# Performance work log

Measured on AMD Instinct MI355X. Metric: run time of the kernel, lower is better.

## Reference

```python
import jax, jax.numpy as jnp
import numpy as np

B = 256          # graphs
NPG = 512        # nodes per graph
N = B * NPG      # 131072 nodes
DEG = 16
E = N * DEG      # 2097152 edges
EPG = E // B
EMB = 256
EF = 8
HID = 32
LATENT = [HID, HID, HID, 1]
TOTAL = sum(LATENT)          # 97
K = 30
S = 5            # max_seq_len
V = 5000         # num_vocab
NT = 100         # node types
ND = 20          # max depth
C1, C2, KW2 = 16, 32, 5
DENSE = ((K - 2) // 2 + 1 - KW2 + 1) * C2  # 352


def glorot(key, shape):
    fan_in, fan_out = shape[0], shape[1]
    lim = np.sqrt(6.0 / (fan_in + fan_out))
    return jax.random.uniform(key, shape, jnp.float32, -lim, lim)


def setup_inputs() -> dict:
    key = jax.random.key(0)
    ks = jax.random.split(key, 24)
    node_type = jax.random.randint(ks[0], (N,), 0, NT)
    node_depth = jax.random.randint(ks[1], (N,), 0, ND)
    # within-graph random edges
    local = jax.random.randint(ks[2], (2, E), 0, NPG)
    gid = jnp.arange(E) // EPG
    edge_index = local + (gid * NPG)[None, :]
    edge_attr = jax.random.normal(ks[3], (E, EF), jnp.float32)
    batch = jnp.arange(N) // NPG
    node_emb = jax.random.normal(ks[4], (NT, EMB), jnp.float32) * 0.02
    depth_emb = jax.random.normal(ks[5], (ND, EMB), jnp.float32) * 0.02
    dims = [(EMB + EF, LATENT[0])] + [(LATENT[i - 1], LATENT[i]) for i in range(1, 4)]
    inp = dict(node_type=node_type, node_depth=node_depth, edge_index=edge_index,
               edge_attr=edge_attr, batch=batch, node_emb=node_emb, depth_emb=depth_emb)
    for i, (di, do) in enumerate(dims):
        inp[f'W{i}'] = glorot(ks[6 + i], (di, do))
        inp[f'b{i}'] = jnp.zeros((do,), jnp.float32)
    inp['conv1_w'] = jax.random.normal(ks[12], (C1, 1, TOTAL), jnp.float32) * 0.05
    inp['conv1_b'] = jnp.zeros((C1,), jnp.float32)
    inp['conv2_w'] = jax.random.normal(ks[13], (C2, C1, KW2), jnp.float32) * 0.05
    inp['conv2_b'] = jnp.zeros((C2,), jnp.float32)
    inp['pred_w'] = glorot(ks[14], (DENSE, V))[None].repeat(S, 0) * 0 + jnp.stack(
        [glorot(jax.random.fold_in(ks[14], i), (DENSE, V)) for i in range(S)])
    inp['pred_b'] = jnp.zeros((S, V), jnp.float32)
    return inp


def _gcn(x, src, dst, W, b):
    # PyG GCNConv: add self-loops, deg over targets, sym-norm, aggregate at dst
    s = jnp.concatenate([src, jnp.arange(N)])
    d = jnp.concatenate([dst, jnp.arange(N)])
    deg = jax.ops.segment_sum(jnp.ones_like(d, jnp.float32), d, num_segments=N)
    dis = jnp.where(deg > 0, 1.0 / jnp.sqrt(deg), 0.0)
    h = x @ W
    norm = dis[s] * dis[d]
    out = jax.ops.segment_sum(h[s] * norm[:, None], d, num_segments=N)
    return out + b


def _forward(node_type, node_depth, edge_index, edge_attr,
             node_emb, depth_emb, W0, b0, W1, b1, W2, b2, W3, b3,
             conv1_w, conv1_b, conv2_w, conv2_b, pred_w, pred_b):
    x = node_emb[node_type] + depth_emb[node_depth]
    src, dst = edge_index[0], edge_index[1]
    # dense e2n scatter matrix @ edge_feat == scatter-add of edge feats to both
    # endpoints; self-loop edges (src==dst) counted once (scatter_ overwrite)
    e2n = jax.ops.segment_sum(edge_attr, src, num_segments=N) + \
          jax.ops.segment_sum(jnp.where((dst != src)[:, None], edge_attr, 0.0), dst, num_segments=N)
    h = jnp.concatenate([x, e2n], axis=1)
    feats = []
    for W, b in ((W0, b0), (W1, b1), (W2, b2), (W3, b3)):
        h = jnp.tanh(_gcn(h, src, dst, W, b))
        feats.append(h)
    msg = jnp.concatenate(feats, axis=1)          # [N, 97]
    # sort pooling: per-graph sort desc by last channel, take top-k
    g = msg.reshape(B, NPG, TOTAL)
    order = jnp.argsort(-g[:, :, -1], axis=1)[:, :K]        # [B, K]
    pooled = jnp.take_along_axis(g, order[:, :, None], axis=1)  # [B, K, 97]
    t = pooled.reshape(B, 1, K * TOTAL)
    dn = ('NCH', 'OIH', 'NCH')
    c = jax.lax.conv_general_dilated(t, conv1_w, (TOTAL,), 'VALID', dimension_numbers=dn)
    c = jax.nn.relu(c + conv1_b[None, :, None])             # [B, 16, 30]
    c = jax.lax.reduce_window(c, -jnp.inf, jax.lax.max, (1, 1, 2), (1, 1, 2), 'VALID')
    c = jax.lax.conv_general_dilated(c, conv2_w, (1,), 'VALID', dimension_numbers=dn)
    c = jax.nn.relu(c + conv2_b[None, :, None])             # [B, 32, 11]
    dense = c.reshape(B, -1)                                # [B, 352]
    preds = jnp.einsum('bd,sdv->sbv', dense, pred_w) + pred_b[:, None, :]
    return preds                                            # [S, B, V]


def reference(node_type, node_depth, edge_index, edge_attr, batch,
              node_emb, depth_emb, W0, b0, W1, b1, W2, b2, W3, b3,
              conv1_w, conv1_b, conv2_w, conv2_b, pred_w, pred_b):
    del batch  # equal-sized graphs: batch structure encoded in reshape
    return _forward(node_type, node_depth, edge_index, edge_attr,
                    node_emb, depth_emb, W0, b0, W1, b1, W2, b2, W3, b3,
                    conv1_w, conv1_b, conv2_w, conv2_b, pred_w, pred_b)
```

## Files before the change

### kernel.cpp

```cpp
#include <hip/hip_runtime.h>

typedef unsigned short ushort_t;

constexpr int cN     = 131072;
constexpr int cE     = 2097152;
constexpr int cB     = 256;
constexpr int cNPG   = 512;
constexpr int cEPG   = 8192;
constexpr int cTOT   = 97;
constexpr int cK     = 30;
constexpr int cV     = 5000;
constexpr int cDENSE = 352;

#define FMA4(A, S, W) \
    (A).x = fmaf((S), (W).x, (A).x); (A).y = fmaf((S), (W).y, (A).y); \
    (A).z = fmaf((S), (W).z, (A).z); (A).w = fmaf((S), (W).w, (A).w)

#define MULADD4(A, X, NRM) \
    (A).x = __fadd_rn((A).x, __fmul_rn((X).x, (NRM))); \
    (A).y = __fadd_rn((A).y, __fmul_rn((X).y, (NRM))); \
    (A).z = __fadd_rn((A).z, __fmul_rn((X).z, (NRM))); \
    (A).w = __fadd_rn((A).w, __fmul_rn((X).w, (NRM)))

__global__ __launch_bounds__(512, 1)
void prep_kernel(const int* __restrict__ ei, const float* __restrict__ attr,
                 float* __restrict__ e2n, float* __restrict__ dis,
                 ushort_t* __restrict__ in_src_g, int* __restrict__ in_off_g)
{
    __shared__ unsigned s_in[cEPG];
    __shared__ ushort_t s_out[cEPG];
    __shared__ int cnt[cNPG];
    __shared__ int woff[cNPG];
    const int g = blockIdx.x, tid = threadIdx.x;
    const int ebase = g * cEPG, nbase = g * cNPG;

    cnt[tid] = 0;
    __syncthreads();

    int er[16];
    #pragma unroll
    for (int j = 0; j < 16; ++j) {
        const int e  = tid + 512 * j;
        const int ls = ei[ebase + e]      - nbase;
        const int ld = ei[cE + ebase + e] - nbase;
        er[j] = ls | (ld << 16);
        atomicAdd(&cnt[ld], 65536);
        atomicAdd(&cnt[ls], 1);
    }
    __syncthreads();

    const int mycnt = cnt[tid];
    int run = mycnt;
    for (int d = 1; d < 512; d <<= 1) {
        const int add = (tid >= d) ? cnt[tid - d] : 0;
        __syncthreads();
        run += add;
        cnt[tid] = run;
        __syncthreads();
    }
    const int myexcl = run - mycnt;
    woff[tid] = myexcl;
    __syncthreads();

    #pragma unroll
    for (int j = 0; j < 16; ++j) {
        const int e  = tid + 512 * j;
        const int ls = er[j] & 0xffff;
        const int ld = er[j] >> 16;
        const int o1 = atomicAdd(&woff[ld], 65536);
        s_in[o1 >> 16] = ((unsigned)e << 16) | (unsigned)ls;
        const int o2 = atomicAdd(&woff[ls], 1);
        s_out[o2 & 0xffff] = (ushort_t)e;
    }
    __syncthreads();

    const int beg_in  = myexcl >> 16,     deg_in  = mycnt >> 16;
    const int beg_out = myexcl & 0xffff,  deg_out = mycnt & 0xffff;

    for (int j = beg_in + 1; j < beg_in + deg_in; ++j) {
        const unsigned x = s_in[j];
        int k = j - 1;
        while (k >= beg_in && s_in[k] > x) { s_in[k + 1] = s_in[k]; --k; }
        s_in[k + 1] = x;
    }
    for (int j = beg_out + 1; j < beg_out + deg_out; ++j) {
        const ushort_t x = s_out[j];
        int k = j - 1;
        while (k >= beg_out && s_out[k] > x) { s_out[k + 1] = s_out[k]; --k; }
        s_out[k + 1] = x;
    }
    __syncthreads();

    float s1[8] = {0,0,0,0,0,0,0,0}, s2[8] = {0,0,0,0,0,0,0,0};
    for (int j = 0; j < deg_out; ++j) {
        const int eid = s_out[beg_out + j];
        const float4* ap = (const float4*)(attr + (size_t)(ebase + eid) * 8);
        const float4 x0 = ap[0], x1 = ap[1];
        s1[0] = __fadd_rn(s1[0], x0.x); s1[1] = __fadd_rn(s1[1], x0.y);
        s1[2] = __fadd_rn(s1[2], x0.z); s1[3] = __fadd_rn(s1[3], x0.w);
        s1[4] = __fadd_rn(s1[4], x1.x); s1[5] = __fadd_rn(s1[5], x1.y);
        s1[6] = __fadd_rn(s1[6], x1.z); s1[7] = __fadd_rn(s1[7], x1.w);
    }
    for (int j = 0; j < deg_in; ++j) {
        const unsigned v = s_in[beg_in + j];
        if ((int)(v & 0xffffu) != tid) {
            const int eid = (int)(v >> 16);
            const float4* ap = (const float4*)(attr + (size_t)(ebase + eid) * 8);
            const float4 x0 = ap[0], x1 = ap[1];
            s2[0] = __fadd_rn(s2[0], x0.x); s2[1] = __fadd_rn(s2[1], x0.y);
            s2[2] = __fadd_rn(s2[2], x0.z); s2[3] = __fadd_rn(s2[3], x0.w);
            s2[4] = __fadd_rn(s2[4], x1.x); s2[5] = __fadd_rn(s2[5], x1.y);
            s2[6] = __fadd_rn(s2[6], x1.z); s2[7] = __fadd_rn(s2[7], x1.w);
        }
    }
    float* eo = e2n + (size_t)(nbase + tid) * 8;
    #pragma unroll
    for (int c = 0; c < 8; ++c) eo[c] = __fadd_rn(s1[c], s2[c]);
    dis[nbase + tid] = 1.0f / sqrtf(1.0f + (float)deg_in);

    {
        unsigned* dst = (unsigned*)(in_src_g + (size_t)g * cEPG);
        for (int i = tid; i < cEPG / 2; i += 512)
            dst[i] = (s_in[2 * i] & 0xffffu) | ((s_in[2 * i + 1] & 0xffffu) << 16);
        in_off_g[g * 513 + tid] = beg_in;
        if (tid == 511) in_off_g[g * 513 + 512] = cEPG;
    }
}

__global__ __launch_bounds__(64, 1)
void tede2_kernel(const float* __restrict__ ne, const float* __restrict__ de,
                  const float* __restrict__ W0, float* __restrict__ T2)
{
    const int combo = blockIdx.x * 2 + (threadIdx.x >> 5);
    const int c = threadIdx.x & 31;
    const int ty = combo / 20, dp = combo - ty * 20;
    const float* np_ = ne + (size_t)ty * 256;
    const float* dd_ = de + (size_t)dp * 256;
    float a = 0.f;
    for (int k = 0; k < 256; ++k)
        a = fmaf(__fadd_rn(np_[k], dd_[k]), W0[k * 32 + c], a);
    T2[(size_t)combo * 32 + c] = a;
}

template<int LAYER>
__global__ __launch_bounds__(512, 1)
void gcn_layer_k(const float* __restrict__ hprev, const float* __restrict__ Wg,
                 const float* __restrict__ bias, const float* __restrict__ dis,
                 const ushort_t* __restrict__ in_src, const int* __restrict__ in_off,
                 float* __restrict__ hout, float* __restrict__ msg,
                 const int* __restrict__ ntype, const int* __restrict__ ndepth,
                 const float* __restrict__ e2n, const float* __restrict__ T2,
                 int* __restrict__ order)
{
    constexpr bool THIN = (LAYER == 3);
    constexpr int USTR = THIN ? 1 : 36;
    extern __shared__ float smem[];
    float* u    = smem;
    float* disl = smem + 512 * USTR;
    int* offl   = (int*)(disl + 512);
    ushort_t* srcl = (ushort_t*)(offl + 516);
    float* key  = (float*)(srcl + cEPG);
    const int g = blockIdx.x, tid = threadIdx.x;
    const int n = g * cNPG + tid;

    {
        const uint4* s4 = (const uint4*)(in_src + (size_t)g * cEPG);
        uint4* d4 = (uint4*)srcl;
        for (int i = tid; i < cEPG / 8; i += 512) d4[i] = s4[i];
        offl[tid] = in_off[g * 513 + tid];
        if (tid == 0) offl[512] = cEPG;
    }
    const float dvd = dis[n];
    disl[tid] = dvd;

    if (!THIN) {
        float hw[32];
        if (LAYER == 0) {
            const int ty = ntype[n], dp = ndepth[n];
            float er[8];
            {
                const float4* ep = (const float4*)(e2n + (size_t)n * 8);
                const float4 x0 = ep[0], x1 = ep[1];
                er[0]=x0.x; er[1]=x0.y; er[2]=x0.z; er[3]=x0.w;
                er[4]=x1.x; er[5]=x1.y; er[6]=x1.z; er[7]=x1.w;
            }
            const float4* tp = (const float4*)(T2 + (size_t)(ty * 20 + dp) * 32);
            #pragma unroll
            for (int cq = 0; cq < 8; ++cq) {
                float4 a = tp[cq];
                #pragma unroll
                for (int f = 0; f < 8; ++f) {
                    const float4 wv = *(const float4*)(Wg + (256 + f) * 32 + cq * 4);
                    FMA4(a, er[f], wv);
                }
                hw[cq*4+0]=a.x; hw[cq*4+1]=a.y; hw[cq*4+2]=a.z; hw[cq*4+3]=a.w;
            }
        } else {
            float hr[32];
            const float4* hp = (const float4*)(hprev + (size_t)n * 32);
            #pragma unroll
            for (int q = 0; q < 8; ++q) {
                const float4 x = hp[q];
                hr[q*4+0]=x.x; hr[q*4+1]=x.y; hr[q*4+2]=x.z; hr[q*4+3]=x.w;
            }
            #pragma unroll
            for (int cq = 0; cq < 8; ++cq) {
                float4 a = {0.f, 0.f, 0.f, 0.f};
                #pragma unroll
                for (int k = 0; k < 32; ++k) {
                    const float4 wv = *(const float4*)(Wg + k * 32 + cq * 4);
                    FMA4(a, hr[k], wv);
                }
                hw[cq*4+0]=a.x; hw[cq*4+1]=a.y; hw[cq*4+2]=a.z; hw[cq*4+3]=a.w;
            }
        }
        {
            float4* up = (float4*)(u + tid * 36);
            #pragma unroll
            for (int cq = 0; cq < 8; ++cq) {
                float4 o; o.x=hw[cq*4+0]; o.y=hw[cq*4+1];
                o.z=hw[cq*4+2]; o.w=hw[cq*4+3];
                up[cq] = o;
            }
        }
        __syncthreads();

        float4 acc[8];
        #pragma unroll
        for (int cq = 0; cq < 8; ++cq) acc[cq] = {0.f, 0.f, 0.f, 0.f};
        const int beg = offl[tid], dnum = offl[tid + 1] - beg;
        for (int j = 0; j < dnum; ++j) {
            const int s = srcl[beg + j];
            const float norm = __fmul_rn(disl[s], dvd);
            const float4* up = (const float4*)(u + s * 36);
            #pragma unroll
            for (int cq = 0; cq < 8; ++cq) {
                const float4 x = up[cq];
                MULADD4(acc[cq], x, norm);
            }
        }
        {
            const float normS = __fmul_rn(dvd, dvd);
            const float4* up = (const float4*)(u + tid * 36);
            #pragma unroll
            for (int cq = 0; cq < 8; ++cq) {
                const float4 x = up[cq];
                MULADD4(acc[cq], x, normS);
            }
        }

        float outv[32];
        #pragma unroll
        for (int cq = 0; cq < 8; ++cq) {
            const float4 bv = *(const float4*)(bias + cq * 4);
            outv[cq*4+0] = (float)tanh((double)__fadd_rn(acc[cq].x, bv.x));
            outv[cq*4+1] = (float)tanh((double)__fadd_rn(acc[cq].y, bv.y));
            outv[cq*4+2] = (float)tanh((double)__fadd_rn(acc[cq].z, bv.z));
            outv[cq*4+3] = (float)tanh((double)__fadd_rn(acc[cq].w, bv.w));
        }
        float4* ho = (float4*)(hout + (size_t)n * 32);
        #pragma unroll
        for (int cq = 0; cq < 8; ++cq) {
            float4 o; o.x = outv[cq*4+0]; o.y = outv[cq*4+1];
            o.z = outv[cq*4+2]; o.w = outv[cq*4+3];
            ho[cq] = o;
        }
        float* mrow = msg + (size_t)n * cTOT + LAYER * 32;
        #pragma unroll
        for (int c = 0; c < 32; ++c) mrow[c] = outv[c];
    } else {
        float hr[32];
        const float4* hp = (const float4*)(hprev + (size_t)n * 32);
        #pragma unroll
        for (int q = 0; q < 8; ++q) {
            const float4 x = hp[q];
            hr[q*4+0]=x.x; hr[q*4+1]=x.y; hr[q*4+2]=x.z; hr[q*4+3]=x.w;
        }
        float s_ = 0.f;
        #pragma unroll
        for (int k = 0; k < 32; ++k) s_ = fmaf(hr[k], Wg[k], s_);
        u[tid] = s_;
        __syncthreads();
        const int beg = offl[tid], dnum = offl[tid + 1] - beg;
        float gs = 0.f;
        for (int j = 0; j < dnum; ++j) {
            const int s = srcl[beg + j];
            gs = __fadd_rn(gs, __fmul_rn(u[s], __fmul_rn(disl[s], dvd)));
        }
        gs = __fadd_rn(gs, __fmul_rn(u[tid], __fmul_rn(dvd, dvd)));
        const float o = (float)tanh((double)__fadd_rn(gs, bias[0]));
        msg[(size_t)n * cTOT + 96] = o;
        key[tid] = o;
        __syncthreads();
        int rank = 0;
        for (int jj = 0; jj < 128; ++jj) {
            const float4 kq = *(const float4*)(key + jj * 4);
            rank += (kq.x > o) || (kq.x == o && (jj*4+0) < tid);
            rank += (kq.y > o) || (kq.y == o && (jj*4+1) < tid);
            rank += (kq.z > o) || (kq.z == o && (jj*4+2) < tid);
            rank += (kq.w > o) || (kq.w == o && (jj*4+3) < tid);
        }
        if (rank < cK) order[g * cK + rank] = n;
    }
}

__global__ __launch_bounds__(512, 1)
void head_kernel(const float* __restrict__ msg, const int* __restrict__ order,
                 const float* __restrict__ c1w, const float* __restrict__ c1b,
                 const float* __restrict__ c2w, const float* __restrict__ c2b,
                 float* __restrict__ dense)
{
    __shared__ float P[cK * cTOT];
    __shared__ float w1[16 * cTOT];
    __shared__ float w2[32 * 16 * 5];
    __shared__ float bb[48];
    __shared__ float Cb[16 * 30];
    __shared__ float Mb[16 * 15];
    const int g = blockIdx.x, tid = threadIdx.x;
    for (int i = tid; i < cK * cTOT; i += 512) {
        const int r = i / cTOT, ii = i - r * cTOT;
        P[i] = msg[(size_t)order[g * cK + r] * cTOT + ii];
    }
    for (int i = tid; i < 16 * cTOT; i += 512) w1[i] = c1w[i];
    for (int i = tid; i < 2560; i += 512) w2[i] = c2w[i];
    if (tid < 16) bb[tid] = c1b[tid];
    else if (tid < 48) bb[tid] = c2b[tid - 16];
    __syncthreads();
    if (tid < 480) {
        const int o = tid / 30, k = tid - o * 30;
        float s = bb[o];
        for (int i = 0; i < cTOT; ++i) s = fmaf(P[k * cTOT + i], w1[o * cTOT + i], s);
        Cb[tid] = fmaxf(s, 0.f);
    }
    __syncthreads();
    if (tid < 240) {
        const int o = tid / 15, p = tid - o * 15;
        Mb[tid] = fmaxf(Cb[o * 30 + 2 * p], Cb[o * 30 + 2 * p + 1]);
    }
    __syncthreads();
    if (tid < cDENSE) {
        const int o2 = tid / 11, q = tid - o2 * 11;
        float s = bb[16 + o2];
        #pragma unroll
        for (int i = 0; i < 16; ++i)
            #pragma unroll
            for (int w = 0; w < 5; ++w)
                s = fmaf(Mb[i * 15 + q + w], w2[(o2 * 16 + i) * 5 + w], s);
        dense[(size_t)g * cDENSE + tid] = fmaxf(s, 0.f);
    }
}

__global__ __launch_bounds__(256, 1)
void pred_gemm_k(const float* __restrict__ dense, const float* __restrict__ pw,
                 const float* __restrict__ pb, float* __restrict__ out)
{
    int w = threadIdx.x >> 6;
    w = __builtin_amdgcn_readfirstlane(w);
    const int lane = threadIdx.x & 63;
    const int s = blockIdx.z, b0 = blockIdx.y * 64;
    const int v = blockIdx.x * 256 + lane * 4;
    if (v >= cV) return;

    const float* dB = dense + (size_t)(b0 + w * 16) * cDENSE;
    const float* wp = pw + (size_t)s * cDENSE * cV + v;

    float4 acc[16];
    #pragma unroll
    for (int bi = 0; bi < 16; ++bi) acc[bi] = {0.f, 0.f, 0.f, 0.f};

    for (int k = 0; k < cDENSE; k += 4) {
        const float* wk = wp + (size_t)k * cV;
        const float4 w0 = *(const float4*)(wk);
        const float4 w1 = *(const float4*)(wk + cV);
        const float4 w2 = *(const float4*)(wk + 2 * cV);
        const float4 w3 = *(const float4*)(wk + 3 * cV);
        #pragma unroll
        for (int bi = 0; bi < 16; ++bi) {
            const float4 dq = *(const float4*)(dB + bi * cDENSE + k);
            FMA4(acc[bi], dq.x, w0);
            FMA4(acc[bi], dq.y, w1);
            FMA4(acc[bi], dq.z, w2);
            FMA4(acc[bi], dq.w, w3);
        }
    }
    const float4 pbv = *(const float4*)(pb + (size_t)s * cV + v);
    #pragma unroll
    for (int bi = 0; bi < 16; ++bi) {
        float4 o;
        o.x = acc[bi].x + pbv.x; o.y = acc[bi].y + pbv.y;
        o.z = acc[bi].z + pbv.z; o.w = acc[bi].w + pbv.w;
        *(float4*)(out + ((size_t)s * cB + b0 + w * 16 + bi) * cV + v) = o;
    }
}

extern "C" void kernel_launch(void* const* d_in, const int* in_sizes, int n_in,
                              void* d_out, int out_size, void* d_ws, size_t ws_size,
                              hipStream_t stream)
{
    const int*   node_type  = (const int*)  d_in[0];
    const int*   node_depth = (const int*)  d_in[1];
    const int*   edge_index = (const int*)  d_in[2];
    const float* edge_attr  = (const float*)d_in[3];
    const float* node_emb   = (const float*)d_in[5];
    const float* depth_emb  = (const float*)d_in[6];
    const float* W0 = (const float*)d_in[7];  const float* b0 = (const float*)d_in[8];
    const float* W1 = (const float*)d_in[9];  const float* b1 = (const float*)d_in[10];
    const float* W2 = (const float*)d_in[11]; const float* b2 = (const float*)d_in[12];
    const float* W3 = (const float*)d_in[13]; const float* b3 = (const float*)d_in[14];
    const float* c1w = (const float*)d_in[15]; const float* c1b = (const float*)d_in[16];
    const float* c2w = (const float*)d_in[17]; const float* c2b = (const float*)d_in[18];
    const float* pw  = (const float*)d_in[19]; const float* pb  = (const float*)d_in[20];
    float* out = (float*)d_out;

    char* p = (char*)d_ws;
    auto carve = [&](size_t bytes) { void* r = (void*)p; p += (bytes + 255) & ~(size_t)255; return r; };
    float*    e2n    = (float*)   carve((size_t)cN * 8 * 4);
    float*    dis    = (float*)   carve((size_t)cN * 4);
    ushort_t* in_src = (ushort_t*)carve((size_t)cE * 2);
    int*      in_off = (int*)     carve((size_t)cB * 513 * 4);
    float*    h      = (float*)   carve((size_t)cN * 32 * 4);
    float*    msg    = (float*)   carve((size_t)cN * cTOT * 4);
    int*      order  = (int*)     carve((size_t)cB * cK * 4);
    float*    dense  = (float*)   carve((size_t)cB * cDENSE * 4);
    float*    T2     = (float*)   carve((size_t)2000 * 32 * 4);

    const int LDS_FAT  = (512 * 36 + 512 + 516) * 4 + cEPG * 2;
    const int LDS_THIN = (512 + 512 + 516) * 4 + cEPG * 2 + 512 * 4;
    hipFuncSetAttribute((const void*)&gcn_layer_k<0>,
                        hipFuncAttributeMaxDynamicSharedMemorySize, LDS_FAT);
    hipFuncSetAttribute((const void*)&gcn_layer_k<1>,
                        hipFuncAttributeMaxDynamicSharedMemorySize, LDS_FAT);
    hipFuncSetAttribute((const void*)&gcn_layer_k<2>,
                        hipFuncAttributeMaxDynamicSharedMemorySize, LDS_FAT);

    tede2_kernel<<<1000, 64, 0, stream>>>(node_emb, depth_emb, W0, T2);
    prep_kernel<<<cB, 512, 0, stream>>>(edge_index, edge_attr, e2n, dis, in_src, in_off);
    gcn_layer_k<0><<<cB, 512, LDS_FAT, stream>>>(nullptr, W0, b0, dis, in_src, in_off,
                                                 h, msg, node_type, node_depth, e2n, T2, nullptr);
    gcn_layer_k<1><<<cB, 512, LDS_FAT, stream>>>(h, W1, b1, dis, in_src, in_off,
                                                 h, msg, nullptr, nullptr, nullptr, nullptr, nullptr);
    gcn_layer_k<2><<<cB, 512, LDS_FAT, stream>>>(h, W2, b2, dis, in_src, in_off,
                                                 h, msg, nullptr, nullptr, nullptr, nullptr, nullptr);
    gcn_layer_k<3><<<cB, 512, LDS_THIN, stream>>>(h, W3, b3, dis, in_src, in_off,
                                                  nullptr, msg, nullptr, nullptr, nullptr, nullptr, order);
    head_kernel<<<cB, 512, 0, stream>>>(msg, order, c1w, c1b, c2w, c2b, dense);
    pred_gemm_k<<<dim3(20, 4, 5), 256, 0, stream>>>(dense, pw, pb, out);
    (void)in_sizes; (void)n_in; (void)out_size; (void)ws_size;
}
```

Baseline: 558.2 us.

## Rewrite prediction GEMM with LDS-tiled 64x128 blocks and 4x8 register tiles

```diff
diff --git a/kernel.cpp b/kernel.cpp
--- a/kernel.cpp
+++ b/kernel.cpp
@@ -350,46 +350,90 @@
     }
 }
 
-__global__ __launch_bounds__(256, 1)
+__global__ __launch_bounds__(256, 4)
 void pred_gemm_k(const float* __restrict__ dense, const float* __restrict__ pw,
                  const float* __restrict__ pb, float* __restrict__ out)
 {
-    int w = threadIdx.x >> 6;
-    w = __builtin_amdgcn_readfirstlane(w);
-    const int lane = threadIdx.x & 63;
-    const int s = blockIdx.z, b0 = blockIdx.y * 64;
-    const int v = blockIdx.x * 256 + lane * 4;
-    if (v >= cV) return;
-
-    const float* dB = dense + (size_t)(b0 + w * 16) * cDENSE;
-    const float* wp = pw + (size_t)s * cDENSE * cV + v;
-
-    float4 acc[16];
+    __shared__ float As[32][68];
+    __shared__ float Bs[32][128];
+    const int s  = blockIdx.z;
+    const int b0 = blockIdx.y * 64;
+    const int vn = blockIdx.x * 128;
+    const int tid = threadIdx.x;
+    const int tm = tid >> 4, tn = tid & 15;
+    const float* wbase = pw + (size_t)s * cDENSE * cV;
+
+    const int ar = tid >> 2;
+    const int ak = (tid & 3) * 8;
+    const int bk = tid >> 3;
+    const int bv = (tid & 7) * 16;
+
+    float4 acc[4][2];
     #pragma unroll
-    for (int bi = 0; bi < 16; ++bi) acc[bi] = {0.f, 0.f, 0.f, 0.f};
-
-    for (int k = 0; k < cDENSE; k += 4) {
-        const float* wk = wp + (size_t)k * cV;
-        const float4 w0 = *(const float4*)(wk);
-        const float4 w1 = *(const float4*)(wk + cV);
-        const float4 w2 = *(const float4*)(wk + 2 * cV);
-        const float4 w3 = *(const float4*)(wk + 3 * cV);
-        #pragma unroll
-        for (int bi = 0; bi < 16; ++bi) {
-            const float4 dq = *(const float4*)(dB + bi * cDENSE + k);
-            FMA4(acc[bi], dq.x, w0);
-            FMA4(acc[bi], dq.y, w1);
-            FMA4(acc[bi], dq.z, w2);
-            FMA4(acc[bi], dq.w, w3);
-        }
-    }
-    const float4 pbv = *(const float4*)(pb + (size_t)s * cV + v);
-    #pragma unroll
-    for (int bi = 0; bi < 16; ++bi) {
-        float4 o;
-        o.x = acc[bi].x + pbv.x; o.y = acc[bi].y + pbv.y;
-        o.z = acc[bi].z + pbv.z; o.w = acc[bi].w + pbv.w;
-        *(float4*)(out + ((size_t)s * cB + b0 + w * 16 + bi) * cV + v) = o;
+    for (int mi = 0; mi < 4; ++mi) {
+        acc[mi][0] = {0.f, 0.f, 0.f, 0.f};
+        acc[mi][1] = {0.f, 0.f, 0.f, 0.f};
+    }
+
+    for (int ks = 0; ks < cDENSE; ks += 32) {
+        const float* arow = dense + (size_t)(b0 + ar) * cDENSE + ks + ak;
+        const float4 a0 = *(const float4*)(arow);
+        const float4 a1 = *(const float4*)(arow + 4);
+        float4 bq[4];
+        {
+            const int gv = vn + bv;
+            const float* brow = wbase + (size_t)(ks + bk) * cV + gv;
+            if (gv + 16 <= cV) {
+                #pragma unroll
+                for (int q = 0; q < 4; ++q) bq[q] = *(const float4*)(brow + q * 4);
+            } else {
+                #pragma unroll
+                for (int q = 0; q < 4; ++q) {
+                    #pragma unroll
+                    for (int j = 0; j < 4; ++j) {
+                        const int vv = gv + q * 4 + j;
+                        ((float*)&bq[q])[j] = (vv < cV) ? brow[q * 4 + j] : 0.f;
+                    }
+                }
+            }
+        }
+        __syncthreads();
+        As[ak + 0][ar] = a0.x; As[ak + 1][ar] = a0.y;
+        As[ak + 2][ar] = a0.z; As[ak + 3][ar] = a0.w;
+        As[ak + 4][ar] = a1.x; As[ak + 5][ar] = a1.y;
+        As[ak + 6][ar] = a1.z; As[ak + 7][ar] = a1.w;
+        #pragma unroll
+        for (int q = 0; q < 4; ++q)
+            *(float4*)(&Bs[bk][bv + q * 4]) = bq[q];
+        __syncthreads();
+        #pragma unroll
+        for (int kk = 0; kk < 32; ++kk) {
+            const float4 av  = *(const float4*)(&As[kk][tm * 4]);
+            const float4 bv0 = *(const float4*)(&Bs[kk][tn * 8]);
+            const float4 bv1 = *(const float4*)(&Bs[kk][tn * 8 + 4]);
+            FMA4(acc[0][0], av.x, bv0); FMA4(acc[0][1], av.x, bv1);
+            FMA4(acc[1][0], av.y, bv0); FMA4(acc[1][1], av.y, bv1);
+            FMA4(acc[2][0], av.z, bv0); FMA4(acc[2][1], av.z, bv1);
+            FMA4(acc[3][0], av.w, bv0); FMA4(acc[3][1], av.w, bv1);
+        }
+    }
+
+    const int gv0 = vn + tn * 8;
+    if (gv0 < cV) {
+        const float4 pb0 = *(const float4*)(pb + (size_t)s * cV + gv0);
+        const float4 pb1 = *(const float4*)(pb + (size_t)s * cV + gv0 + 4);
+        #pragma unroll
+        for (int mi = 0; mi < 4; ++mi) {
+            const int row = b0 + tm * 4 + mi;
+            float* op = out + ((size_t)s * cB + row) * cV + gv0;
+            float4 o0, o1;
+            o0.x = acc[mi][0].x + pb0.x; o0.y = acc[mi][0].y + pb0.y;
+            o0.z = acc[mi][0].z + pb0.z; o0.w = acc[mi][0].w + pb0.w;
+            o1.x = acc[mi][1].x + pb1.x; o1.y = acc[mi][1].y + pb1.y;
+            o1.z = acc[mi][1].z + pb1.z; o1.w = acc[mi][1].w + pb1.w;
+            *(float4*)(op)     = o0;
+            *(float4*)(op + 4) = o1;
+        }
     }
 }
 
@@ -444,6 +488,6 @@
     gcn_layer_k<3><<<cB, 512, LDS_THIN, stream>>>(h, W3, b3, dis, in_src, in_off,
                                                   nullptr, msg, nullptr, nullptr, nullptr, nullptr, order);
     head_kernel<<<cB, 512, 0, stream>>>(msg, order, c1w, c1b, c2w, c2b, dense);
-    pred_gemm_k<<<dim3(20, 4, 5), 256, 0, stream>>>(dense, pw, pb, out);
+    pred_gemm_k<<<dim3(40, 4, 5), 256, 0, stream>>>(dense, pw, pb, out);
     (void)in_sizes; (void)n_in; (void)out_size; (void)ws_size;
 }
```

Result: faster. 492.4 us (-11.8%).
